# Kernel optimization log

Hardware: AMD Instinct MI355X
Metric: run time of the kernel (lower is better)

The kernel has to match this reference:

```python
import jax, jax.numpy as jnp
import numpy as np

N_NODES = 100000
N_EDGES = 1600000
NUM_FEATURES = 100
HIDDEN = 32
OUT = 2
DROP_P = 0.2


def setup_inputs() -> dict:
    key = jax.random.key(0)
    ks = jax.random.split(key, 6)
    x = jax.random.normal(ks[0], (N_NODES, NUM_FEATURES), dtype=jnp.float32)
    edge_index = jax.random.randint(ks[1], (2, N_EDGES), 0, N_NODES, dtype=jnp.int64)
    # Glorot-ish init for weights
    W1 = jax.random.normal(ks[2], (NUM_FEATURES, HIDDEN), dtype=jnp.float32) / jnp.sqrt(NUM_FEATURES)
    b1 = jnp.zeros((HIDDEN,), dtype=jnp.float32)
    W2 = jax.random.normal(ks[3], (HIDDEN, OUT), dtype=jnp.float32) / jnp.sqrt(HIDDEN)
    b2 = jnp.zeros((OUT,), dtype=jnp.float32)
    return {"x": x, "edge_index": edge_index, "W1": W1, "b1": b1, "W2": W2, "b2": b2}


def _gcn_norm(edge_index, num_nodes):
    # add self loops (fixed-size concat -> jit friendly)
    loops = jnp.arange(num_nodes, dtype=edge_index.dtype)
    src = jnp.concatenate([edge_index[0], loops])
    dst = jnp.concatenate([edge_index[1], loops])
    deg = jax.ops.segment_sum(jnp.ones_like(dst, dtype=jnp.float32), dst, num_segments=num_nodes)
    dinv = jnp.where(deg > 0, jax.lax.rsqrt(deg), 0.0)
    norm = dinv[src] * dinv[dst]  # [E+N]
    return src, dst, norm


def _gcn_conv(x, W, b, src, dst, norm, num_nodes):
    h = x @ W  # [N, d_out]
    msg = h[src] * norm[:, None]  # gather + scale
    out = jax.ops.segment_sum(msg, dst, num_segments=num_nodes)  # scatter-add
    return out + b


def reference(x, edge_index, W1, b1, W2, b2):
    n = x.shape[0]
    src, dst, norm = _gcn_norm(edge_index, n)
    h = jax.nn.relu(_gcn_conv(x, W1, b1, src, dst, norm, n))
    # deterministic dropout (p=0.2) with fixed key, inverted scaling as in F.dropout
    keep = jax.random.bernoulli(jax.random.key(42), 1.0 - DROP_P, h.shape)
    h = jnp.where(keep, h / (1.0 - DROP_P), 0.0)
    logits = _gcn_conv(h, W2, b2, src, dst, norm, n)
    return jax.nn.log_softmax(logits, axis=1)
```

## Files before the change

### kernel.cpp

```cpp
#include <hip/hip_runtime.h>
#include <stdint.h>
#include <math.h>

#define N_NODES   100000
#define N_EDGES   1600000
#define NFEAT     100
#define HIDDEN    32
#define OUTC      2

#define BUCK_BITS 7
#define BUCK_SZ   128
#define NBUCK     782
#define PADB      4096

#define PART_NB   256
#define PART_CHUNK ((N_EDGES + PART_NB - 1) / PART_NB)
#define PART_SLOTS 7
#define SORT_SLOTS 16

typedef float fx4 __attribute__((ext_vector_type(4)));

__device__ __forceinline__ uint32_t rotl32(uint32_t x, int r) {
    return (x << r) | (x >> (32 - r));
}

__device__ __forceinline__ uint32_t threefry_bits(uint32_t f) {
    const uint32_t ks0 = 0u;
    const uint32_t ks1 = 42u;
    const uint32_t ks2 = 0x1BD11BDAu ^ 0u ^ 42u;
    uint32_t x0 = 0u + ks0;
    uint32_t x1 = f  + ks1;
#define TF_ROUND(r) { x0 += x1; x1 = rotl32(x1, (r)); x1 ^= x0; }
    TF_ROUND(13) TF_ROUND(15) TF_ROUND(26) TF_ROUND(6)
    x0 += ks1; x1 += ks2 + 1u;
    TF_ROUND(17) TF_ROUND(29) TF_ROUND(16) TF_ROUND(24)
    x0 += ks2; x1 += ks0 + 2u;
    TF_ROUND(13) TF_ROUND(15) TF_ROUND(26) TF_ROUND(6)
    x0 += ks0; x1 += ks1 + 3u;
    TF_ROUND(17) TF_ROUND(29) TF_ROUND(16) TF_ROUND(24)
    x0 += ks1; x1 += ks2 + 4u;
    TF_ROUND(13) TF_ROUND(15) TF_ROUND(26) TF_ROUND(6)
    x0 += ks2; x1 += ks0 + 5u;
#undef TF_ROUND
    return x0 ^ x1;
}

__device__ __forceinline__ bool dropout_keep(uint32_t f) {
    uint32_t bits = threefry_bits(f);
    float u = __uint_as_float((bits >> 9) | 0x3f800000u) - 1.0f;
    return u < 0.8f;
}

__device__ __forceinline__ uint16_t f2bf(float f) {
    uint32_t b = __float_as_uint(f);
    uint32_t lsb = (b >> 16) & 1u;
    b += 0x7fffu + lsb;
    return (uint16_t)(b >> 16);
}
__device__ __forceinline__ float bflo(uint32_t u) {
    return __uint_as_float(u << 16);
}
__device__ __forceinline__ float bfhi(uint32_t u) {
    return __uint_as_float(u & 0xffff0000u);
}

__global__ __launch_bounds__(256) void k_init(int* __restrict__ bcur) {
    int i = blockIdx.x * 256 + threadIdx.x;
    if (i < NBUCK) bcur[i] = i * PADB;
}

__global__ __launch_bounds__(1024) void k_part(const int* __restrict__ src,
                                               const int* __restrict__ dst,
                                               int* __restrict__ bcur,
                                               uint32_t* __restrict__ part) {
    __shared__ int h4[4][NBUCK];
    __shared__ int c4[4][NBUCK];
    const int t = threadIdx.x;
    const int w = (t >> 6) & 3;
    const int base = blockIdx.x * PART_CHUNK;
    const int lim = min(base + PART_CHUNK, N_EDGES);
    for (int i = t; i < 4 * NBUCK; i += 1024) ((int*)h4)[i] = 0;
    __syncthreads();
    uint32_t ed[PART_SLOTS];
    int      eb[PART_SLOTS];
#pragma unroll
    for (int k = 0; k < PART_SLOTS; ++k) {
        int e = base + t + k * 1024;
        bool v = e < lim;
        int d = v ? dst[e] : 0;
        int s = v ? src[e] : 0;
        eb[k] = v ? (d >> BUCK_BITS) : -1;
        ed[k] = ((uint32_t)(d & (BUCK_SZ - 1)) << 17) | (uint32_t)s;
        if (v) atomicAdd(&h4[w][d >> BUCK_BITS], 1);
    }
    __syncthreads();
    if (t < NBUCK) {
        int c0 = h4[0][t], c1 = h4[1][t], c2 = h4[2][t], c3 = h4[3][t];
        int tot = c0 + c1 + c2 + c3;
        int g = tot ? atomicAdd(&bcur[t], tot) : 0;
        c4[0][t] = g;
        c4[1][t] = g + c0;
        c4[2][t] = g + c0 + c1;
        c4[3][t] = g + c0 + c1 + c2;
    }
    __syncthreads();
#pragma unroll
    for (int k = 0; k < PART_SLOTS; ++k) {
        if (eb[k] >= 0) {
            int pos = atomicAdd(&c4[w][eb[k]], 1);
            part[pos] = ed[k];
        }
    }
}

__global__ __launch_bounds__(256) void k_sort(const uint32_t* __restrict__ part,
                                              const int* __restrict__ bcur,
                                              int* __restrict__ csr_src,
                                              int* __restrict__ rowbeg,
                                              int* __restrict__ deg,
                                              float* __restrict__ dinv) {
    __shared__ int cnt4[4][BUCK_SZ];
    __shared__ int pref[BUCK_SZ];
    __shared__ int cur4[4][BUCK_SZ];
    const int b = blockIdx.x;
    const int t = threadIdx.x;
    const int w = t >> 6;
    const int nbase = b * BUCK_SZ;
    const int bb = b * PADB;
    const int be = bcur[b];
    for (int i = t; i < 4 * BUCK_SZ; i += 256) ((int*)cnt4)[i] = 0;
    __syncthreads();
    uint32_t ed[SORT_SLOTS];
#pragma unroll
    for (int k = 0; k < SORT_SLOTS; ++k) {
        int j = bb + t + k * 256;
        bool v = j < be;
        uint32_t val = v ? part[j] : 0xFFFFFFFFu;
        ed[k] = val;
        if (v) atomicAdd(&cnt4[w][(val >> 17) & (BUCK_SZ - 1)], 1);
    }
    __syncthreads();
    int c0 = 0, c1 = 0, c2 = 0, tot = 0;
    if (t < BUCK_SZ) {
        c0 = cnt4[0][t]; c1 = cnt4[1][t]; c2 = cnt4[2][t];
        tot = c0 + c1 + c2 + cnt4[3][t];
        pref[t] = tot;
    }
    __syncthreads();
#pragma unroll
    for (int off = 1; off < BUCK_SZ; off <<= 1) {
        int v = (t >= off && t < BUCK_SZ) ? pref[t - off] : 0;
        __syncthreads();
        if (t < BUCK_SZ) pref[t] += v;
        __syncthreads();
    }
    if (t < BUCK_SZ) {
        int ex = pref[t] - tot;
        cur4[0][t] = ex;
        cur4[1][t] = ex + c0;
        cur4[2][t] = ex + c0 + c1;
        cur4[3][t] = ex + c0 + c1 + c2;
        int node = nbase + t;
        if (node < N_NODES) {
            rowbeg[node] = bb + ex;
            deg[node] = tot;
            dinv[node] = rsqrtf((float)(tot + 1));
        }
    }
    __syncthreads();
#pragma unroll
    for (int k = 0; k < SORT_SLOTS; ++k) {
        if (ed[k] != 0xFFFFFFFFu) {
            int dl = (ed[k] >> 17) & (BUCK_SZ - 1);
            int pos = bb + atomicAdd(&cur4[w][dl], 1);
            csr_src[pos] = (int)(ed[k] & 0x1FFFF);
        }
    }
}

__global__ __launch_bounds__(256) void k_gemm1(const float* __restrict__ x,
                                               const float* __restrict__ W1,
                                               const float* __restrict__ dinv,
                                               uint16_t* __restrict__ h0b) {
    __shared__ __align__(16) float w1s[NFEAT * HIDDEN];
    __shared__ __align__(16) float xs[32 * NFEAT];
    const int tid = threadIdx.x;
    for (int i = tid; i < NFEAT * HIDDEN / 4; i += 256)
        ((fx4*)w1s)[i] = ((const fx4*)W1)[i];
    const int row0 = blockIdx.x * 32;
    const fx4* xb = (const fx4*)(x + (size_t)row0 * NFEAT);
    for (int i = tid; i < 800; i += 256)
        ((fx4*)xs)[i] = __builtin_nontemporal_load(&xb[i]);
    __syncthreads();
    const int c = tid & 31, r0 = tid >> 5;
    float a0 = 0.f, a1 = 0.f, a2 = 0.f, a3 = 0.f;
#pragma unroll 4
    for (int k = 0; k < NFEAT; ++k) {
        float wv = w1s[k * HIDDEN + c];
        a0 = fmaf(xs[(r0)      * NFEAT + k], wv, a0);
        a1 = fmaf(xs[(r0 + 8)  * NFEAT + k], wv, a1);
        a2 = fmaf(xs[(r0 + 16) * NFEAT + k], wv, a2);
        a3 = fmaf(xs[(r0 + 24) * NFEAT + k], wv, a3);
    }
    const int r = row0 + r0;
    h0b[(size_t)(r)      * HIDDEN + c] = f2bf(a0 * dinv[r]);
    h0b[(size_t)(r + 8)  * HIDDEN + c] = f2bf(a1 * dinv[r + 8]);
    h0b[(size_t)(r + 16) * HIDDEN + c] = f2bf(a2 * dinv[r + 16]);
    h0b[(size_t)(r + 24) * HIDDEN + c] = f2bf(a3 * dinv[r + 24]);
}

__global__ __launch_bounds__(256) void k_l1(const int* __restrict__ rowbeg,
                                            const int* __restrict__ deg,
                                            const int* __restrict__ csr_src,
                                            const float* __restrict__ dinv,
                                            const uint4* __restrict__ h0u,
                                            const float* __restrict__ b1,
                                            const float* __restrict__ W2,
                                            float* __restrict__ h2s) {
    const int t = blockIdx.x * 256 + threadIdx.x;
    const int n = t >> 2;
    const int l = t & 3;
    if (n >= N_NODES) return;
    uint4 self = h0u[(size_t)n * 4 + l];
    float aL0 = bflo(self.x), aH0 = bfhi(self.x);
    float aL1 = bflo(self.y), aH1 = bfhi(self.y);
    float aL2 = bflo(self.z), aH2 = bfhi(self.z);
    float aL3 = bflo(self.w), aH3 = bfhi(self.w);
    const int beg = rowbeg[n];
    const int d = deg[n];
    const int end = beg + d;
    const int mainEnd = beg + (d & ~3);
    int j = beg;
    int s0, s1, s2, s3;
    if (j < mainEnd) {
        s0 = csr_src[j]; s1 = csr_src[j + 1];
        s2 = csr_src[j + 2]; s3 = csr_src[j + 3];
    }
    for (; j < mainEnd; j += 4) {
        uint4 u0 = h0u[(size_t)s0 * 4 + l];
        uint4 u1 = h0u[(size_t)s1 * 4 + l];
        uint4 u2 = h0u[(size_t)s2 * 4 + l];
        uint4 u3 = h0u[(size_t)s3 * 4 + l];
        int pj = (j + 8 <= mainEnd) ? j + 4 : beg;
        s0 = csr_src[pj];     s1 = csr_src[pj + 1];
        s2 = csr_src[pj + 2]; s3 = csr_src[pj + 3];
        aL0 += bflo(u0.x); aH0 += bfhi(u0.x); aL1 += bflo(u0.y); aH1 += bfhi(u0.y);
        aL2 += bflo(u0.z); aH2 += bfhi(u0.z); aL3 += bflo(u0.w); aH3 += bfhi(u0.w);
        aL0 += bflo(u1.x); aH0 += bfhi(u1.x); aL1 += bflo(u1.y); aH1 += bfhi(u1.y);
        aL2 += bflo(u1.z); aH2 += bfhi(u1.z); aL3 += bflo(u1.w); aH3 += bfhi(u1.w);
        aL0 += bflo(u2.x); aH0 += bfhi(u2.x); aL1 += bflo(u2.y); aH1 += bfhi(u2.y);
        aL2 += bflo(u2.z); aH2 += bfhi(u2.z); aL3 += bflo(u2.w); aH3 += bfhi(u2.w);
        aL0 += bflo(u3.x); aH0 += bfhi(u3.x); aL1 += bflo(u3.y); aH1 += bfhi(u3.y);
        aL2 += bflo(u3.z); aH2 += bfhi(u3.z); aL3 += bflo(u3.w); aH3 += bfhi(u3.w);
    }
    for (; j < end; ++j) {
        uint4 u = h0u[(size_t)csr_src[j] * 4 + l];
        aL0 += bflo(u.x); aH0 += bfhi(u.x); aL1 += bflo(u.y); aH1 += bfhi(u.y);
        aL2 += bflo(u.z); aH2 += bfhi(u.z); aL3 += bflo(u.w); aH3 += bfhi(u.w);
    }
    const int c0 = 8 * l;
    const float din = dinv[n];
    float v0 = fmaxf(fmaf(aL0, din, b1[c0 + 0]), 0.0f);
    float v1 = fmaxf(fmaf(aH0, din, b1[c0 + 1]), 0.0f);
    float v2 = fmaxf(fmaf(aL1, din, b1[c0 + 2]), 0.0f);
    float v3 = fmaxf(fmaf(aH1, din, b1[c0 + 3]), 0.0f);
    float v4 = fmaxf(fmaf(aL2, din, b1[c0 + 4]), 0.0f);
    float v5 = fmaxf(fmaf(aH2, din, b1[c0 + 5]), 0.0f);
    float v6 = fmaxf(fmaf(aL3, din, b1[c0 + 6]), 0.0f);
    float v7 = fmaxf(fmaf(aH3, din, b1[c0 + 7]), 0.0f);
    const uint32_t fb = (uint32_t)(n * HIDDEN + c0);
    v0 = dropout_keep(fb + 0) ? v0 * 1.25f : 0.0f;
    v1 = dropout_keep(fb + 1) ? v1 * 1.25f : 0.0f;
    v2 = dropout_keep(fb + 2) ? v2 * 1.25f : 0.0f;
    v3 = dropout_keep(fb + 3) ? v3 * 1.25f : 0.0f;
    v4 = dropout_keep(fb + 4) ? v4 * 1.25f : 0.0f;
    v5 = dropout_keep(fb + 5) ? v5 * 1.25f : 0.0f;
    v6 = dropout_keep(fb + 6) ? v6 * 1.25f : 0.0f;
    v7 = dropout_keep(fb + 7) ? v7 * 1.25f : 0.0f;
    float p0 = v0 * W2[(c0 + 0) * 2] + v1 * W2[(c0 + 1) * 2]
             + v2 * W2[(c0 + 2) * 2] + v3 * W2[(c0 + 3) * 2]
             + v4 * W2[(c0 + 4) * 2] + v5 * W2[(c0 + 5) * 2]
             + v6 * W2[(c0 + 6) * 2] + v7 * W2[(c0 + 7) * 2];
    float p1 = v0 * W2[(c0 + 0) * 2 + 1] + v1 * W2[(c0 + 1) * 2 + 1]
             + v2 * W2[(c0 + 2) * 2 + 1] + v3 * W2[(c0 + 3) * 2 + 1]
             + v4 * W2[(c0 + 4) * 2 + 1] + v5 * W2[(c0 + 5) * 2 + 1]
             + v6 * W2[(c0 + 6) * 2 + 1] + v7 * W2[(c0 + 7) * 2 + 1];
#pragma unroll
    for (int m = 2; m >= 1; m >>= 1) {
        p0 += __shfl_xor(p0, m);
        p1 += __shfl_xor(p1, m);
    }
    if (l == 0) {
        float2* o = (float2*)(h2s + (size_t)n * 2);
        *o = make_float2(p0 * din, p1 * din);
    }
}

__global__ __launch_bounds__(256) void k_l2(const int* __restrict__ rowbeg,
                                            const int* __restrict__ deg,
                                            const int* __restrict__ csr_src,
                                            const float* __restrict__ dinv,
                                            const float* __restrict__ h2s,
                                            const float* __restrict__ b2,
                                            float* __restrict__ out) {
    int t = blockIdx.x * 256 + threadIdx.x;
    int n = t >> 3;
    int l = t & 7;
    if (n >= N_NODES) return;
    float acc0 = 0.0f, acc1 = 0.0f;
    float bcc0 = 0.0f, bcc1 = 0.0f;
    if (l == 0) {
        float2 hn = ((const float2*)h2s)[n];
        acc0 = hn.x; acc1 = hn.y;
    }
    const int beg = rowbeg[n];
    const int end = beg + deg[n];
    int j = beg + l;
    for (; j + 8 < end; j += 16) {
        int s0 = __builtin_nontemporal_load(&csr_src[j]);
        int s1 = __builtin_nontemporal_load(&csr_src[j + 8]);
        float2 h0v = ((const float2*)h2s)[s0];
        float2 h1v = ((const float2*)h2s)[s1];
        acc0 += h0v.x; acc1 += h0v.y;
        bcc0 += h1v.x; bcc1 += h1v.y;
    }
    if (j < end) {
        float2 hv = ((const float2*)h2s)[__builtin_nontemporal_load(&csr_src[j])];
        acc0 += hv.x; acc1 += hv.y;
    }
    acc0 += bcc0; acc1 += bcc1;
#pragma unroll
    for (int m = 4; m >= 1; m >>= 1) {
        acc0 += __shfl_xor(acc0, m);
        acc1 += __shfl_xor(acc1, m);
    }
    if (l == 0) {
        float din = dinv[n];
        float l0 = fmaf(acc0, din, b2[0]);
        float l1 = fmaf(acc1, din, b2[1]);
        float m = fmaxf(l0, l1);
        float lse = m + logf(expf(l0 - m) + expf(l1 - m));
        float2* o = (float2*)(out + (size_t)n * 2);
        *o = make_float2(l0 - lse, l1 - lse);
    }
}

static inline size_t align_up(size_t x) { return (x + 255) & ~(size_t)255; }

extern "C" void kernel_launch(void* const* d_in, const int* in_sizes, int n_in,
                              void* d_out, int out_size, void* d_ws, size_t ws_size,
                              hipStream_t stream) {
    (void)n_in; (void)in_sizes; (void)out_size; (void)ws_size;

    const float* x  = (const float*)d_in[0];
    const int*   ei = (const int*)d_in[1];
    const float* W1 = (const float*)d_in[2];
    const float* b1 = (const float*)d_in[3];
    const float* W2 = (const float*)d_in[4];
    const float* b2 = (const float*)d_in[5];
    float* out = (float*)d_out;

    const int* src = ei;
    const int* dst = ei + N_EDGES;

    char* w = (char*)d_ws;
    size_t off = 0;
    int*      bcur   = (int*)(w + off);      off += align_up((size_t)NBUCK * 4);
    int*      rowbeg = (int*)(w + off);      off += align_up((size_t)N_NODES * 4);
    int*      deg    = (int*)(w + off);      off += align_up((size_t)N_NODES * 4);
    float*    dinv   = (float*)(w + off);    off += align_up((size_t)N_NODES * 4);
    uint32_t* part   = (uint32_t*)(w + off); off += align_up((size_t)NBUCK * PADB * 4);
    int*      csr    = (int*)(w + off);      off += align_up((size_t)NBUCK * PADB * 4);
    uint16_t* h0b    = (uint16_t*)(w + off); off += align_up((size_t)N_NODES * HIDDEN * 2);
    float*    h2s    = (float*)(w + off);    off += align_up((size_t)N_NODES * OUTC * 4);

    const int B = 256;
    k_init <<<(NBUCK + B - 1) / B, B, 0, stream>>>(bcur);
    k_part <<<PART_NB, 1024, 0, stream>>>(src, dst, bcur, part);
    k_sort <<<NBUCK, B, 0, stream>>>(part, bcur, csr, rowbeg, deg, dinv);
    k_gemm1<<<N_NODES / 32, B, 0, stream>>>(x, W1, dinv, h0b);
    k_l1   <<<(N_NODES * 4 + B - 1) / B, B, 0, stream>>>(rowbeg, deg, csr, dinv, (const uint4*)h0b, b1, W2, h2s);
    k_l2   <<<(N_NODES * 8 + B - 1) / B, B, 0, stream>>>(rowbeg, deg, csr, dinv, h2s, b2, out);
}
```

Before: 181.3 us.

## Pad CSR rows to multiples of eight with a zero dummy node and unroll gathers

Each node's CSR row is padded up to a multiple of 8 entries with the index of an extra dummy node. That node's h0 and h2 rows are zeroed in k_init. The layer-1 gather can then run a tail-free loop unrolled by eight, keeping more independent loads in flight. The layer-2 loop bounds change to match the padding. The k_sort prefix scan is replaced with a wavefront shuffle scan plus one cross-wave add, dropping most block barriers. In exchange, padding adds redundant gathers of the dummy row (cache-resident) and extra CSR writes, and bucket occupancy grows toward PADB.

After: 182.4 us. No clear change (+0.6%).

```diff
diff --git a/kernel.cpp b/kernel.cpp
--- a/kernel.cpp
+++ b/kernel.cpp
@@ -12,6 +12,7 @@
 #define BUCK_SZ   128
 #define NBUCK     782
 #define PADB      4096
+#define DUMMY     N_NODES
 
 #define PART_NB   256
 #define PART_CHUNK ((N_EDGES + PART_NB - 1) / PART_NB)
@@ -64,9 +65,13 @@
     return __uint_as_float(u & 0xffff0000u);
 }
 
-__global__ __launch_bounds__(256) void k_init(int* __restrict__ bcur) {
+__global__ __launch_bounds__(256) void k_init(int* __restrict__ bcur,
+                                              uint32_t* __restrict__ h0d,
+                                              float* __restrict__ h2d) {
     int i = blockIdx.x * 256 + threadIdx.x;
     if (i < NBUCK) bcur[i] = i * PADB;
+    if (i < 16) h0d[(size_t)DUMMY * 16 + i] = 0u;
+    if (i >= 16 && i < 18) h2d[(size_t)DUMMY * 2 + (i - 16)] = 0.0f;
 }
 
 __global__ __launch_bounds__(1024) void k_part(const int* __restrict__ src,
@@ -120,8 +125,8 @@
                                               int* __restrict__ deg,
                                               float* __restrict__ dinv) {
     __shared__ int cnt4[4][BUCK_SZ];
-    __shared__ int pref[BUCK_SZ];
     __shared__ int cur4[4][BUCK_SZ];
+    __shared__ int w0tot;
     const int b = blockIdx.x;
     const int t = threadIdx.x;
     const int w = t >> 6;
@@ -140,22 +145,24 @@
         if (v) atomicAdd(&cnt4[w][(val >> 17) & (BUCK_SZ - 1)], 1);
     }
     __syncthreads();
-    int c0 = 0, c1 = 0, c2 = 0, tot = 0;
+    int c0 = 0, c1 = 0, c2 = 0, tot = 0, ptot = 0;
     if (t < BUCK_SZ) {
         c0 = cnt4[0][t]; c1 = cnt4[1][t]; c2 = cnt4[2][t];
         tot = c0 + c1 + c2 + cnt4[3][t];
-        pref[t] = tot;
-    }
-    __syncthreads();
-#pragma unroll
-    for (int off = 1; off < BUCK_SZ; off <<= 1) {
-        int v = (t >= off && t < BUCK_SZ) ? pref[t - off] : 0;
-        __syncthreads();
-        if (t < BUCK_SZ) pref[t] += v;
-        __syncthreads();
-    }
+        ptot = (tot + 7) & ~7;
+    }
+    int s = ptot;
+    const int lane = t & 63;
+#pragma unroll
+    for (int o = 1; o < 64; o <<= 1) {
+        int x = __shfl_up(s, o);
+        if (lane >= o) s += x;
+    }
+    if (t == 63) w0tot = s;
+    __syncthreads();
+    if (t >= 64 && t < BUCK_SZ) s += w0tot;
     if (t < BUCK_SZ) {
-        int ex = pref[t] - tot;
+        int ex = s - ptot;
         cur4[0][t] = ex;
         cur4[1][t] = ex + c0;
         cur4[2][t] = ex + c0 + c1;
@@ -166,6 +173,7 @@
             deg[node] = tot;
             dinv[node] = rsqrtf((float)(tot + 1));
         }
+        for (int i = tot; i < ptot; ++i) csr_src[bb + ex + i] = DUMMY;
     }
     __syncthreads();
 #pragma unroll
@@ -228,22 +236,29 @@
     float aL3 = bflo(self.w), aH3 = bfhi(self.w);
     const int beg = rowbeg[n];
     const int d = deg[n];
-    const int end = beg + d;
-    const int mainEnd = beg + (d & ~3);
+    const int end8 = beg + ((d + 7) & ~7);
     int j = beg;
-    int s0, s1, s2, s3;
-    if (j < mainEnd) {
-        s0 = csr_src[j]; s1 = csr_src[j + 1];
+    int s0, s1, s2, s3, s4, s5, s6, s7;
+    if (j < end8) {
+        s0 = csr_src[j];     s1 = csr_src[j + 1];
         s2 = csr_src[j + 2]; s3 = csr_src[j + 3];
-    }
-    for (; j < mainEnd; j += 4) {
+        s4 = csr_src[j + 4]; s5 = csr_src[j + 5];
+        s6 = csr_src[j + 6]; s7 = csr_src[j + 7];
+    }
+    for (; j < end8; j += 8) {
         uint4 u0 = h0u[(size_t)s0 * 4 + l];
         uint4 u1 = h0u[(size_t)s1 * 4 + l];
         uint4 u2 = h0u[(size_t)s2 * 4 + l];
         uint4 u3 = h0u[(size_t)s3 * 4 + l];
-        int pj = (j + 8 <= mainEnd) ? j + 4 : beg;
+        uint4 u4 = h0u[(size_t)s4 * 4 + l];
+        uint4 u5 = h0u[(size_t)s5 * 4 + l];
+        uint4 u6 = h0u[(size_t)s6 * 4 + l];
+        uint4 u7 = h0u[(size_t)s7 * 4 + l];
+        int pj = (j + 16 <= end8) ? j + 8 : beg;
         s0 = csr_src[pj];     s1 = csr_src[pj + 1];
         s2 = csr_src[pj + 2]; s3 = csr_src[pj + 3];
+        s4 = csr_src[pj + 4]; s5 = csr_src[pj + 5];
+        s6 = csr_src[pj + 6]; s7 = csr_src[pj + 7];
         aL0 += bflo(u0.x); aH0 += bfhi(u0.x); aL1 += bflo(u0.y); aH1 += bfhi(u0.y);
         aL2 += bflo(u0.z); aH2 += bfhi(u0.z); aL3 += bflo(u0.w); aH3 += bfhi(u0.w);
         aL0 += bflo(u1.x); aH0 += bfhi(u1.x); aL1 += bflo(u1.y); aH1 += bfhi(u1.y);
@@ -252,11 +267,14 @@
         aL2 += bflo(u2.z); aH2 += bfhi(u2.z); aL3 += bflo(u2.w); aH3 += bfhi(u2.w);
         aL0 += bflo(u3.x); aH0 += bfhi(u3.x); aL1 += bflo(u3.y); aH1 += bfhi(u3.y);
         aL2 += bflo(u3.z); aH2 += bfhi(u3.z); aL3 += bflo(u3.w); aH3 += bfhi(u3.w);
-    }
-    for (; j < end; ++j) {
-        uint4 u = h0u[(size_t)csr_src[j] * 4 + l];
-        aL0 += bflo(u.x); aH0 += bfhi(u.x); aL1 += bflo(u.y); aH1 += bfhi(u.y);
-        aL2 += bflo(u.z); aH2 += bfhi(u.z); aL3 += bflo(u.w); aH3 += bfhi(u.w);
+        aL0 += bflo(u4.x); aH0 += bfhi(u4.x); aL1 += bflo(u4.y); aH1 += bfhi(u4.y);
+        aL2 += bflo(u4.z); aH2 += bfhi(u4.z); aL3 += bflo(u4.w); aH3 += bfhi(u4.w);
+        aL0 += bflo(u5.x); aH0 += bfhi(u5.x); aL1 += bflo(u5.y); aH1 += bfhi(u5.y);
+        aL2 += bflo(u5.z); aH2 += bfhi(u5.z); aL3 += bflo(u5.w); aH3 += bfhi(u5.w);
+        aL0 += bflo(u6.x); aH0 += bfhi(u6.x); aL1 += bflo(u6.y); aH1 += bfhi(u6.y);
+        aL2 += bflo(u6.z); aH2 += bfhi(u6.z); aL3 += bflo(u6.w); aH3 += bfhi(u6.w);
+        aL0 += bflo(u7.x); aH0 += bfhi(u7.x); aL1 += bflo(u7.y); aH1 += bfhi(u7.y);
+        aL2 += bflo(u7.z); aH2 += bfhi(u7.z); aL3 += bflo(u7.w); aH3 += bfhi(u7.w);
     }
     const int c0 = 8 * l;
     const float din = dinv[n];
@@ -314,9 +332,9 @@
         acc0 = hn.x; acc1 = hn.y;
     }
     const int beg = rowbeg[n];
-    const int end = beg + deg[n];
+    const int end8 = beg + ((deg[n] + 7) & ~7);
     int j = beg + l;
-    for (; j + 8 < end; j += 16) {
+    for (; j + 8 < end8; j += 16) {
         int s0 = __builtin_nontemporal_load(&csr_src[j]);
         int s1 = __builtin_nontemporal_load(&csr_src[j + 8]);
         float2 h0v = ((const float2*)h2s)[s0];
@@ -324,7 +342,7 @@
         acc0 += h0v.x; acc1 += h0v.y;
         bcc0 += h1v.x; bcc1 += h1v.y;
     }
-    if (j < end) {
+    if (j < end8) {
         float2 hv = ((const float2*)h2s)[__builtin_nontemporal_load(&csr_src[j])];
         acc0 += hv.x; acc1 += hv.y;
     }
@@ -371,11 +389,11 @@
     float*    dinv   = (float*)(w + off);    off += align_up((size_t)N_NODES * 4);
     uint32_t* part   = (uint32_t*)(w + off); off += align_up((size_t)NBUCK * PADB * 4);
     int*      csr    = (int*)(w + off);      off += align_up((size_t)NBUCK * PADB * 4);
-    uint16_t* h0b    = (uint16_t*)(w + off); off += align_up((size_t)N_NODES * HIDDEN * 2);
-    float*    h2s    = (float*)(w + off);    off += align_up((size_t)N_NODES * OUTC * 4);
+    uint16_t* h0b    = (uint16_t*)(w + off); off += align_up((size_t)(N_NODES + 1) * HIDDEN * 2);
+    float*    h2s    = (float*)(w + off);    off += align_up((size_t)(N_NODES + 1) * OUTC * 4);
 
     const int B = 256;
-    k_init <<<(NBUCK + B - 1) / B, B, 0, stream>>>(bcur);
+    k_init <<<(NBUCK + B - 1) / B, B, 0, stream>>>(bcur, (uint32_t*)h0b, h2s);
     k_part <<<PART_NB, 1024, 0, stream>>>(src, dst, bcur, part);
     k_sort <<<NBUCK, B, 0, stream>>>(part, bcur, csr, rowbeg, deg, dinv);
     k_gemm1<<<N_NODES / 32, B, 0, stream>>>(x, W1, dinv, h0b);
```
